# Optimization experiments

Measured on AMD Instinct MI355X. Metric: run time of the kernel, lower is better.

## Reference

```python
import jax, jax.numpy as jnp
import numpy as np
from jax import lax

N_NODES = 20000
N_EDGES = 320000
FEAT = 100
N_RULES = 64
T_RULE = 50
H_RNN = 256
RULE_NUMS = 16
NTN_OUT = 200


def setup_inputs() -> dict:
    key = jax.random.key(0)
    ks = iter(jax.random.split(key, 64))
    nrm = lambda shape, s=0.05: jax.random.normal(next(ks), shape, jnp.float32) * s
    inp = {}
    inp["node_features_0"] = jax.random.normal(next(ks), (N_NODES, FEAT), jnp.float32)
    inp["node_features_1"] = jax.random.normal(next(ks), (N_NODES, FEAT), jnp.float32)
    inp["edge_indices_0"] = jax.random.randint(next(ks), (2, N_EDGES), 0, N_NODES)
    inp["edge_indices_1"] = jax.random.randint(next(ks), (2, N_EDGES), 0, N_NODES)
    inp["edge_features_0"] = jax.random.normal(next(ks), (N_EDGES, FEAT), jnp.float32)
    inp["edge_features_1"] = jax.random.normal(next(ks), (N_EDGES, FEAT), jnp.float32)
    inp["rules"] = jax.random.normal(next(ks), (N_RULES, T_RULE, FEAT), jnp.float32)
    # TripleConv 1: edge lin (3*100 -> 100) and nn = mlp (100->100->100)
    inp["c1_lin_W"] = nrm((FEAT, 3 * FEAT)); inp["c1_lin_b"] = jnp.zeros((FEAT,))
    inp["c1_W1"] = nrm((FEAT, FEAT)); inp["c1_b1"] = jnp.zeros((FEAT,))
    inp["c1_W2"] = nrm((FEAT, FEAT)); inp["c1_b2"] = jnp.zeros((FEAT,))
    # TripleConv 2
    inp["c2_lin_W"] = nrm((FEAT, 3 * FEAT)); inp["c2_lin_b"] = jnp.zeros((FEAT,))
    inp["c2_W1"] = nrm((FEAT, FEAT)); inp["c2_b1"] = jnp.zeros((FEAT,))
    inp["c2_W2"] = nrm((FEAT, FEAT)); inp["c2_b2"] = jnp.zeros((FEAT,))
    # NTN (input_dim=100 to match pooled graph vectors, out_dim=200)
    inp["ntn_W"] = nrm((FEAT, FEAT, NTN_OUT))
    inp["ntn_V"] = nrm((NTN_OUT, 2 * FEAT))
    inp["ntn_B"] = jnp.zeros((NTN_OUT,))
    # RuleEmbedding: 2-layer tanh RNN (100 -> 256 -> 256) + Linear(256,100)
    inp["rnn0_Wih"] = nrm((H_RNN, FEAT)); inp["rnn0_Whh"] = nrm((H_RNN, H_RNN))
    inp["rnn0_bih"] = jnp.zeros((H_RNN,)); inp["rnn0_bhh"] = jnp.zeros((H_RNN,))
    inp["rnn1_Wih"] = nrm((H_RNN, H_RNN)); inp["rnn1_Whh"] = nrm((H_RNN, H_RNN))
    inp["rnn1_bih"] = jnp.zeros((H_RNN,)); inp["rnn1_bhh"] = jnp.zeros((H_RNN,))
    inp["rule_lin_W"] = nrm((FEAT, H_RNN)); inp["rule_lin_b"] = jnp.zeros((FEAT,))
    # RuleRanker 100->128->64->1
    inp["rk_W1"] = nrm((128, FEAT)); inp["rk_b1"] = jnp.zeros((128,))
    inp["rk_W2"] = nrm((64, 128)); inp["rk_b2"] = jnp.zeros((64,))
    inp["rk_W3"] = nrm((1, 64)); inp["rk_b3"] = jnp.zeros((1,))
    # Head: fc1 (200 + rule_nums*100 -> 500) -> fc2 (500->100) -> fc3 (100->1)
    inp["fc1_W"] = nrm((500, NTN_OUT + RULE_NUMS * FEAT)); inp["fc1_b"] = jnp.zeros((500,))
    inp["fc2_W"] = nrm((FEAT, 500)); inp["fc2_b"] = jnp.zeros((FEAT,))
    inp["fc3_W"] = nrm((1, FEAT)); inp["fc3_b"] = jnp.zeros((1,))
    return inp


def _triple_conv(x, src, dst, e, lin_W, lin_b, W1, b1, W2, b2):
    # message: relu(Linear(concat(x_i, edge_attr, x_j))); PyG: i=target, j=source
    m = jax.nn.relu(jnp.concatenate([x[dst], e, x[src]], axis=1) @ lin_W.T + lin_b)
    agg = jax.ops.segment_sum(m, dst, num_segments=x.shape[0])  # aggr='add'
    out = agg + x  # (1 + eps) * x_r with eps = 0
    h = jax.nn.relu(out @ W1.T + b1)
    return h @ W2.T + b2  # nn = Sequential(Linear, ReLU, Linear)


def _conv_pass(x, ei, e, c_lin_W, c_lin_b, c_W1, c_b1, c_W2, c_b2,
               d_lin_W, d_lin_b, d_W1, d_b1, d_W2, d_b2):
    src, dst = ei[0], ei[1]
    x = jax.nn.relu(_triple_conv(x, src, dst, e, c_lin_W, c_lin_b, c_W1, c_b1, c_W2, c_b2))
    x = jax.nn.relu(_triple_conv(x, src, dst, e, d_lin_W, d_lin_b, d_W1, d_b1, d_W2, d_b2))
    return x


def _rnn_layer(x_tbf, Wih, Whh, bih, bhh):
    # x_tbf: [T, B, in]; returns all hidden states [T, B, H] and final [B, H]
    h0 = jnp.zeros((x_tbf.shape[1], Whh.shape[0]), x_tbf.dtype)
    def step(h, xt):
        h = jnp.tanh(xt @ Wih.T + bih + h @ Whh.T + bhh)
        return h, h
    hT, ys = lax.scan(step, h0, x_tbf)
    return ys, hT


def reference(node_features_0, node_features_1, edge_indices_0, edge_indices_1,
              edge_features_0, edge_features_1, rules,
              c1_lin_W, c1_lin_b, c1_W1, c1_b1, c1_W2, c1_b2,
              c2_lin_W, c2_lin_b, c2_W1, c2_b1, c2_W2, c2_b2,
              ntn_W, ntn_V, ntn_B,
              rnn0_Wih, rnn0_Whh, rnn0_bih, rnn0_bhh,
              rnn1_Wih, rnn1_Whh, rnn1_bih, rnn1_bhh,
              rule_lin_W, rule_lin_b,
              rk_W1, rk_b1, rk_W2, rk_b2, rk_W3, rk_b3,
              fc1_W, fc1_b, fc2_W, fc2_b, fc3_W, fc3_b):
    # --- rule embedding (all sequences full length => pack/pad is identity) ---
    x = jnp.transpose(rules, (1, 0, 2))  # [T, B, 100]
    ys, _ = _rnn_layer(x, rnn0_Wih, rnn0_Whh, rnn0_bih, rnn0_bhh)
    _, hT = _rnn_layer(ys, rnn1_Wih, rnn1_Whh, rnn1_bih, rnn1_bhh)
    rules_embedding = hT @ rule_lin_W.T + rule_lin_b  # [B, 100]
    # --- rule ranking + top-k ---
    h = jax.nn.relu(rules_embedding @ rk_W1.T + rk_b1)
    h = jax.nn.relu(h @ rk_W2.T + rk_b2)
    rules_score = jax.nn.sigmoid(h @ rk_W3.T + rk_b3)[:, 0]  # [B]
    _, top_idx = lax.top_k(rules_score, RULE_NUMS)
    top_rules_embedding = rules_embedding[top_idx]  # [rule_nums, 100]
    # --- GNN message passing on both graphs ---
    f1 = _conv_pass(node_features_0, edge_indices_0, edge_features_0,
                    c1_lin_W, c1_lin_b, c1_W1, c1_b1, c1_W2, c1_b2,
                    c2_lin_W, c2_lin_b, c2_W1, c2_b1, c2_W2, c2_b2)
    f2 = _conv_pass(node_features_1, edge_indices_1, edge_features_1,
                    c1_lin_W, c1_lin_b, c1_W1, c1_b1, c1_W2, c1_b2,
                    c2_lin_W, c2_lin_b, c2_W1, c2_b1, c2_W2, c2_b2)
    g1 = jnp.sum(f1, axis=0, keepdims=True)  # global_add_pool, single graph -> [1, 100]
    g2 = jnp.sum(f2, axis=0, keepdims=True)
    # --- NTN(g1, g2) ---
    tp = jnp.einsum('ai,ijk,bj->abk', g1, ntn_W, g2)  # [1,1,200]
    concat = jnp.concatenate([g1[:, None, :] * jnp.ones_like(g2)[None, :, :1],
                              g2[None, :, :] * jnp.ones_like(g1)[:, None, :1]], axis=2)
    lin_term = concat @ ntn_V.T  # [1,1,200]
    ntn_out = jax.nn.relu(tp + lin_term + ntn_B).reshape(-1)  # squeeze -> [200]
    # --- scoring head ---
    feat = jnp.concatenate([ntn_out, top_rules_embedding.reshape(-1)])  # [200 + rule_nums*100]
    z = jax.nn.relu(feat @ fc1_W.T + fc1_b)
    z = jax.nn.relu(z @ fc2_W.T + fc2_b)
    score = jax.nn.sigmoid(z @ fc3_W.T + fc3_b)
    return score.reshape(())
```

## Files before the change

### kernel.cpp

```cpp
#include <hip/hip_runtime.h>

typedef unsigned short u16;
typedef unsigned int u32;

#define N_NODES 20000
#define N_EDGES 320000
#define FEAT 100
#define XPAD 112
#define N_RULES 64
#define T_RULE 50
#define H_RNN 256
#define RULE_NUMS 16
#define NTN_OUT 200
#define SCAN_B 79
#define NPB 16

typedef __attribute__((ext_vector_type(8))) short short8;
typedef __attribute__((ext_vector_type(4))) float f32x4;

__device__ __forceinline__ u16 f2bu(float f) {
  u32 u = __float_as_uint(f);
  u32 r = (u + 0x7fffu + ((u >> 16) & 1u)) >> 16;
  return (u16)r;
}
__device__ __forceinline__ float bu2f(u16 u) {
  return __uint_as_float(((u32)u) << 16);
}
__device__ __forceinline__ u32 pk2(float a, float b) {
  return (u32)f2bu(a) | ((u32)f2bu(b) << 16);
}

__device__ __forceinline__ void lds_st16(void* base, int byteOff, uint4 v) {
  *(uint4*)((char*)base + byteOff) = v;
}
__device__ __forceinline__ short8 lds_ld16(const void* base, int byteOff) {
  return *(const short8*)((const char*)base + byteOff);
}

#define SWZ(row, kByte) (((((row) << 8) + (kByte))) ^ (((row) & 7) << 4))

__device__ __forceinline__ int hs_off(int row, int chunk) {
  return (row << 9) | (((chunk + row * 5) & 31) << 4);
}

__device__ __forceinline__ float tanh_fast(float x) {
  const float e = __expf(2.f * x);
  return 1.f - 2.f / (e + 1.f);
}

__global__ void k_prep(const float* __restrict__ nf0, const float* __restrict__ nf1,
                       u16* __restrict__ xb0, u16* __restrict__ xb1) {
  const int total = N_NODES * XPAD;
  for (int i = blockIdx.x * blockDim.x + threadIdx.x; i < total;
       i += gridDim.x * blockDim.x) {
    const int n = i / XPAD;
    const int c = i - n * XPAD;
    const float v0 = (c < FEAT) ? nf0[(size_t)n * FEAT + c] : 0.f;
    const float v1 = (c < FEAT) ? nf1[(size_t)n * FEAT + c] : 0.f;
    xb0[i] = f2bu(v0);
    xb1[i] = f2bu(v1);
  }
}

__global__ void k_wprep(const float* __restrict__ linW, u16* __restrict__ Wb) {
  const int idx = blockIdx.x * blockDim.x + threadIdx.x;
  if (idx >= 3 * 128 * 128) return;
  const int c = idx >> 14;
  const int rem = idx & 16383;
  const int r = rem >> 7;
  const int k = rem & 127;
  u16 v = 0;
  if (r < FEAT && k < FEAT) v = f2bu(linW[(size_t)r * 300 + c * 100 + k]);
  Wb[idx] = v;
}

__global__ void k_wprep_sq(const float* __restrict__ W, u16* __restrict__ Wb) {
  const int idx = blockIdx.x * blockDim.x + threadIdx.x;
  if (idx >= 128 * 128) return;
  const int r = idx >> 7;
  const int k = idx & 127;
  u16 v = 0;
  if (r < FEAT && k < FEAT) v = f2bu(W[(size_t)r * FEAT + k]);
  Wb[idx] = v;
}

__global__ void k_count2(const int* __restrict__ d0, const int* __restrict__ d1,
                         int* __restrict__ cnt) {
  const int e = blockIdx.x * blockDim.x + threadIdx.x;
  const int* d = blockIdx.y ? d1 : d0;
  if (e < N_EDGES) atomicAdd(&cnt[blockIdx.y * N_NODES + d[e]], 1);
}

__global__ __launch_bounds__(256) void k_scan1(const int* __restrict__ cnt,
                                               int* __restrict__ off,
                                               int* __restrict__ bsum) {
  __shared__ int buf[256];
  const int g = blockIdx.y, b = blockIdx.x, tid = threadIdx.x;
  const int i = b * 256 + tid;
  const int v = (i < N_NODES) ? cnt[g * N_NODES + i] : 0;
  buf[tid] = v;
  __syncthreads();
  for (int ofs = 1; ofs < 256; ofs <<= 1) {
    const int t = (tid >= ofs) ? buf[tid - ofs] : 0;
    __syncthreads();
    buf[tid] += t;
    __syncthreads();
  }
  if (i < N_NODES) off[g * (N_NODES + 1) + i] = buf[tid] - v;
  if (tid == 255) bsum[g * SCAN_B + b] = buf[255];
}

__global__ __launch_bounds__(128) void k_scan2(int* __restrict__ bsum) {
  __shared__ int s[128];
  const int g = blockIdx.y, tid = threadIdx.x;
  const int v = (tid < SCAN_B) ? bsum[g * SCAN_B + tid] : 0;
  s[tid] = v;
  __syncthreads();
  for (int ofs = 1; ofs < 128; ofs <<= 1) {
    const int t = (tid >= ofs) ? s[tid - ofs] : 0;
    __syncthreads();
    s[tid] += t;
    __syncthreads();
  }
  if (tid < SCAN_B) bsum[g * SCAN_B + tid] = s[tid] - v;
}

__global__ __launch_bounds__(256) void k_scan3(const int* __restrict__ bsum,
                                               int* __restrict__ off,
                                               int* __restrict__ cursor) {
  const int g = blockIdx.y, b = blockIdx.x, tid = threadIdx.x;
  const int i = b * 256 + tid;
  if (i < N_NODES) {
    const int o = off[g * (N_NODES + 1) + i] + bsum[g * SCAN_B + b];
    off[g * (N_NODES + 1) + i] = o;
    cursor[g * N_NODES + i] = o;
  }
  if (i == N_NODES) off[g * (N_NODES + 1) + N_NODES] = N_EDGES;
}

__global__ void k_scatter2(const int* __restrict__ s0, const int* __restrict__ d0,
                           const int* __restrict__ s1, const int* __restrict__ d1,
                           int* __restrict__ cursor,
                           int* __restrict__ el0, int* __restrict__ el1,
                           int* __restrict__ sp0, int* __restrict__ sp1,
                           int* __restrict__ dp0, int* __restrict__ dp1) {
  const int e = blockIdx.x * blockDim.x + threadIdx.x;
  const int g = blockIdx.y;
  const int* d = g ? d1 : d0;
  const int* s = g ? s1 : s0;
  if (e < N_EDGES) {
    const int dn = d[e];
    const int pos = atomicAdd(&cursor[g * N_NODES + dn], 1);
    (g ? el1 : el0)[pos] = e;
    (g ? sp1 : sp0)[pos] = s[e];
    (g ? dp1 : dp0)[pos] = dn;
  }
}

template <int VARIANT>
__global__ __launch_bounds__(256) void k_gemm_u(
    const float* __restrict__ Af, const u16* __restrict__ Ab,
    const float* __restrict__ W, const float* __restrict__ b0,
    const float* __restrict__ b1, float* __restrict__ Uout) {
  __shared__ __align__(16) u16 As[64 * 128];
  __shared__ __align__(16) u16 Bs[128 * 128];
  const int tid = threadIdx.x;
  const int lane = tid & 63;
  const int wv = tid >> 6;
  const int l15 = lane & 15;
  const int lhi = lane >> 4;
  const int mb = blockIdx.x * 64;
  const int nb = blockIdx.y * 128;
  const int rb = (wv >> 1) * 32;
  const int cb = (wv & 1) * 64;
  constexpr int KV = VARIANT ? 256 : 100;
  constexpr int NPH = VARIANT ? 2 : 1;

  f32x4 acc[2][4];
  const f32x4 z4 = {0.f, 0.f, 0.f, 0.f};
#pragma unroll
  for (int i = 0; i < 2; ++i)
#pragma unroll
    for (int j = 0; j < 4; ++j) acc[i][j] = z4;

  for (int kc = 0; kc < NPH; ++kc) {
    __syncthreads();
    {
      const int row = tid >> 2;
      const int k0 = (tid & 3) * 32;
      const int gm = mb + row;
      if (VARIANT == 0) {
        const int r = gm & 63;
        const int t = gm >> 6;
        const float* ar = Af + ((size_t)r * T_RULE + t) * FEAT;
#pragma unroll
        for (int c = 0; c < 4; ++c) {
          const int k = k0 + c * 8;
          uint4 v = {0u, 0u, 0u, 0u};
          if (k + 8 <= KV) {
            const float4 fa = *(const float4*)(ar + k);
            const float4 fb = *(const float4*)(ar + k + 4);
            v.x = pk2(fa.x, fa.y); v.y = pk2(fa.z, fa.w);
            v.z = pk2(fb.x, fb.y); v.w = pk2(fb.z, fb.w);
          } else if (k < KV) {
            const float4 fa = *(const float4*)(ar + k);
            v.x = pk2(fa.x, fa.y); v.y = pk2(fa.z, fa.w);
          }
          lds_st16(As, SWZ(row, k * 2), v);
        }
      } else {
        const uint4* ar = (const uint4*)(Ab + (size_t)gm * 256 + kc * 128 + k0);
#pragma unroll
        for (int c = 0; c < 4; ++c)
          lds_st16(As, SWZ(row, (k0 + c * 8) * 2), ar[c]);
      }
    }
    {
      const int row = tid >> 1;
      const int k0 = (tid & 1) * 64;
      const float* wr = W + (size_t)(nb + row) * KV;
#pragma unroll
      for (int c = 0; c < 8; ++c) {
        const int k = k0 + c * 8;
        const int kg = kc * 128 + k;
        uint4 v = {0u, 0u, 0u, 0u};
        if (kg + 8 <= KV) {
          const float4 fa = *(const float4*)(wr + kg);
          const float4 fb = *(const float4*)(wr + kg + 4);
          v.x = pk2(fa.x, fa.y); v.y = pk2(fa.z, fa.w);
          v.z = pk2(fb.x, fb.y); v.w = pk2(fb.z, fb.w);
        } else if (kg < KV) {
          const float4 fa = *(const float4*)(wr + kg);
          v.x = pk2(fa.x, fa.y); v.y = pk2(fa.z, fa.w);
        }
        lds_st16(Bs, SWZ(row, k * 2), v);
      }
    }
    __syncthreads();
#pragma unroll
    for (int s = 0; s < 4; ++s) {
      const int kByte = s * 64 + lhi * 16;
      short8 af[2], bfr[4];
#pragma unroll
      for (int i = 0; i < 2; ++i)
        af[i] = lds_ld16(As, SWZ(rb + i * 16 + l15, kByte));
#pragma unroll
      for (int j = 0; j < 4; ++j)
        bfr[j] = lds_ld16(Bs, SWZ(cb + j * 16 + l15, kByte));
#pragma unroll
      for (int i = 0; i < 2; ++i)
#pragma unroll
        for (int j = 0; j < 4; ++j)
          acc[i][j] = __builtin_amdgcn_mfma_f32_16x16x32_bf16(af[i], bfr[j],
                                                              acc[i][j], 0, 0, 0);
    }
  }
#pragma unroll
  for (int j = 0; j < 4; ++j) {
    const int col = nb + cb + j * 16 + l15;
    const float bias = b0[col] + b1[col];
#pragma unroll
    for (int i = 0; i < 2; ++i) {
      const int base_m = mb + rb + i * 16 + lhi * 4;
      const int t = base_m >> 6;
      const int r0 = base_m & 63;
      float4 st;
      st.x = acc[i][j][0] + bias; st.y = acc[i][j][1] + bias;
      st.z = acc[i][j][2] + bias; st.w = acc[i][j][3] + bias;
      *(float4*)(Uout + ((size_t)t * 256 + col) * 64 + r0) = st;
    }
  }
}

template <int WRITE_YS>
__global__ __launch_bounds__(512) void k_rec(
    const float* __restrict__ U, const float* __restrict__ Whh,
    u16* __restrict__ ys, float* __restrict__ hT) {
  __shared__ __align__(16) u16 Hs[16 * 256];
  const int tid = threadIdx.x;
  const int lane = tid & 63;
  const int wv = tid >> 6;
  const int cbase = wv * 32;
  const int ruleBase = blockIdx.x * 16;
  const int l15 = lane & 15;
  const int lhi = lane >> 4;

  short8 bf[2][8];
#pragma unroll
  for (int jt = 0; jt < 2; ++jt) {
    const int col = cbase + jt * 16 + l15;
    const float* wr = Whh + (size_t)col * 256;
#pragma unroll
    for (int s = 0; s < 8; ++s) {
      const int k0 = s * 32 + lhi * 8;
      const float4 fa = *(const float4*)(wr + k0);
      const float4 fb = *(const float4*)(wr + k0 + 4);
      uint4 v;
      v.x = pk2(fa.x, fa.y); v.y = pk2(fa.z, fa.w);
      v.z = pk2(fb.x, fb.y); v.w = pk2(fb.z, fb.w);
      bf[jt][s] = *(short8*)&v;
    }
  }
  for (int i = tid; i < 16 * 256 / 8; i += 512) {
    const uint4 z = {0u, 0u, 0u, 0u};
    ((uint4*)Hs)[i] = z;
  }
  __syncthreads();

  const int n0 = cbase + l15;
  const int n1 = cbase + 16 + l15;
  const int m0 = lhi * 4;
  float4 Ua0 = *(const float4*)(U + ((size_t)n0) * 64 + m0);
  float4 Ua1 = *(const float4*)(U + ((size_t)n1) * 64 + m0);

  const f32x4 z4 = {0.f, 0.f, 0.f, 0.f};
  float hv[2][4];
  for (int t = 0; t < T_RULE; ++t) {
    const int tn = (t + 1 < T_RULE) ? t + 1 : t;
    const float4 Ub0 = *(const float4*)(U + ((size_t)tn * 256 + n0) * 64 + m0);
    const float4 Ub1 = *(const float4*)(U + ((size_t)tn * 256 + n1) * 64 + m0);
    f32x4 acc[2] = {z4, z4};
#pragma unroll
    for (int s = 0; s < 8; ++s) {
      const short8 af = lds_ld16(Hs, hs_off(l15, s * 4 + lhi));
      acc[0] = __builtin_amdgcn_mfma_f32_16x16x32_bf16(af, bf[0][s], acc[0], 0, 0, 0);
      acc[1] = __builtin_amdgcn_mfma_f32_16x16x32_bf16(af, bf[1][s], acc[1], 0, 0, 0);
    }
    const float ua0[4] = {Ua0.x, Ua0.y, Ua0.z, Ua0.w};
    const float ua1[4] = {Ua1.x, Ua1.y, Ua1.z, Ua1.w};
#pragma unroll
    for (int q = 0; q < 4; ++q) {
      hv[0][q] = tanh_fast(ua0[q] + acc[0][q]);
      hv[1][q] = tanh_fast(ua1[q] + acc[1][q]);
    }
    __syncthreads();
#pragma unroll
    for (int jt = 0; jt < 2; ++jt) {
      const int n = cbase + jt * 16 + l15;
#pragma unroll
      for (int q = 0; q < 4; ++q) {
        const int m = lhi * 4 + q;
        const u16 hb = f2bu(hv[jt][q]);
        *(u16*)((char*)Hs + (hs_off(m, n >> 3) + ((n & 7) << 1))) = hb;
        if (WRITE_YS)
          ys[(((size_t)t * 64 + ruleBase + m) << 8) + n] = hb;
      }
    }
    Ua0 = Ub0; Ua1 = Ub1;
    __syncthreads();
  }
  if (!WRITE_YS) {
#pragma unroll
    for (int jt = 0; jt < 2; ++jt) {
      const int n = cbase + jt * 16 + l15;
#pragma unroll
      for (int q = 0; q < 4; ++q) {
        const int m = lhi * 4 + q;
        hT[((size_t)(ruleBase + m) << 8) + n] = hv[jt][q];
      }
    }
  }
}

__global__ __launch_bounds__(128) void k_rulelin(
    const float* __restrict__ hT, const float* __restrict__ rlW,
    const float* __restrict__ rlb, float* __restrict__ emb) {
  __shared__ __align__(16) float hs[H_RNN];
  const int b = blockIdx.x;
  const int tid = threadIdx.x;
  for (int i = tid; i < H_RNN / 4; i += 128)
    ((float4*)hs)[i] = ((const float4*)(hT + (size_t)b * H_RNN))[i];
  __syncthreads();
  if (tid < FEAT) {
    float acc = rlb[tid];
    const float4* w = (const float4*)(rlW + (size_t)tid * H_RNN);
    const float4* hv = (const float4*)hs;
#pragma unroll 8
    for (int k = 0; k < 64; ++k) {
      const float4 a = w[k], x = hv[k];
      acc += a.x * x.x + a.y * x.y + a.z * x.z + a.w * x.w;
    }
    emb[(size_t)b * FEAT + tid] = acc;
  }
}

__global__ __launch_bounds__(128) void k_ranker(
    const float* __restrict__ emb,
    const float* __restrict__ W1, const float* __restrict__ b1,
    const float* __restrict__ W2, const float* __restrict__ b2,
    const float* __restrict__ W3, const float* __restrict__ b3,
    float* __restrict__ scores) {
  __shared__ float eb[FEAT];
  __shared__ float h1s[128];
  __shared__ float h2s[64];
  const int r = blockIdx.x;
  const int tid = threadIdx.x;
  if (tid < FEAT) eb[tid] = emb[(size_t)r * FEAT + tid];
  __syncthreads();
  {
    float acc = b1[tid];
    const float* w = W1 + (size_t)tid * FEAT;
    for (int k = 0; k < FEAT; ++k) acc += w[k] * eb[k];
    h1s[tid] = acc > 0.f ? acc : 0.f;
  }
  __syncthreads();
  if (tid < 64) {
    float acc = b2[tid];
    const float* w = W2 + (size_t)tid * 128;
    for (int k = 0; k < 128; ++k) acc += w[k] * h1s[k];
    h2s[tid] = acc > 0.f ? acc : 0.f;
  }
  __syncthreads();
  if (tid == 0) {
    float acc = b3[0];
    for (int k = 0; k < 64; ++k) acc += W3[k] * h2s[k];
    scores[r] = acc;
  }
}

__global__ void k_topk(const float* __restrict__ scores, int* __restrict__ topidx) {
  if (threadIdx.x == 0 && blockIdx.x == 0) {
    float s[N_RULES];
    for (int i = 0; i < N_RULES; ++i) s[i] = scores[i];
    for (int t = 0; t < RULE_NUMS; ++t) {
      int best = 0;
      float bv = s[0];
      for (int i = 1; i < N_RULES; ++i)
        if (s[i] > bv) { bv = s[i]; best = i; }
      topidx[t] = best;
      s[best] = -1e30f;
    }
  }
}

__global__ __launch_bounds__(256) void k_nodegemm(
    const u16* __restrict__ xb, const u16* __restrict__ Wb,
    const float* __restrict__ linB, u16* __restrict__ P, u16* __restrict__ Q) {
  __shared__ __align__(16) u16 As[128 * 128];
  __shared__ __align__(16) u16 Bs[128 * 128];
  const int tid = threadIdx.x;
  const int lane = tid & 63;
  const int wv = tid >> 6;
  const int l15 = lane & 15;
  const int lhi = lane >> 4;
  const int n0 = blockIdx.x * 128;
  const int p = blockIdx.y;
  const int rStage = tid >> 1;
  const int hf = tid & 1;
  const int rb = (wv >> 1) * 64;
  const int cb = (wv & 1) * 64;

  {
    const int node = n0 + rStage;
    const bool ok = node < N_NODES;
    const uint4* xr = (const uint4*)(xb + (size_t)node * XPAD);
#pragma unroll
    for (int q = 0; q < 8; ++q) {
      const int cc = hf * 8 + q;
      uint4 v = {0u, 0u, 0u, 0u};
      if (ok && cc < 14) v = xr[cc];
      lds_st16(As, SWZ(rStage, cc * 16), v);
    }
  }
  {
    const uint4* wr = (const uint4*)(Wb + (size_t)(p ? 2 : 0) * 16384 +
                                     (size_t)rStage * 128);
#pragma unroll
    for (int q = 0; q < 8; ++q) {
      const int cc = hf * 8 + q;
      lds_st16(Bs, SWZ(rStage, cc * 16), wr[cc]);
    }
  }
  __syncthreads();

  f32x4 acc[4][4];
  const f32x4 z4 = {0.f, 0.f, 0.f, 0.f};
#pragma unroll
  for (int i = 0; i < 4; ++i)
#pragma unroll
    for (int j = 0; j < 4; ++j) acc[i][j] = z4;
#pragma unroll
  for (int s = 0; s < 4; ++s) {
    const int kByte = s * 64 + lhi * 16;
    short8 af[4], bfr[4];
#pragma unroll
    for (int i = 0; i < 4; ++i) {
      af[i] = lds_ld16(As, SWZ(rb + i * 16 + l15, kByte));
      bfr[i] = lds_ld16(Bs, SWZ(cb + i * 16 + l15, kByte));
    }
#pragma unroll
    for (int i = 0; i < 4; ++i)
#pragma unroll
      for (int j = 0; j < 4; ++j)
        acc[i][j] = __builtin_amdgcn_mfma_f32_16x16x32_bf16(af[i], bfr[j],
                                                            acc[i][j], 0, 0, 0);
  }
  u16* Out = p ? Q : P;
#pragma unroll
  for (int j = 0; j < 4; ++j) {
    const int col = cb + j * 16 + l15;
    if (col >= XPAD) continue;
    const bool valid = col < FEAT;
    const float bias = (valid && !p) ? linB[col] : 0.f;
#pragma unroll
    for (int i = 0; i < 4; ++i) {
      const int row0 = rb + i * 16 + lhi * 4;
#pragma unroll
      for (int q = 0; q < 4; ++q) {
        const int node = n0 + row0 + q;
        if (node < N_NODES)
          Out[(size_t)node * XPAD + col] = valid ? f2bu(acc[i][j][q] + bias) : (u16)0;
      }
    }
  }
}

__global__ __launch_bounds__(256, 3) void k_msgagg2(
    const float* __restrict__ ef, const u16* __restrict__ Wb,
    const int* __restrict__ elist, const int* __restrict__ spos,
    const int* __restrict__ dpos, const int* __restrict__ off,
    const u16* __restrict__ Pb, const u16* __restrict__ Qb,
    const u16* __restrict__ xb, u16* __restrict__ aggb) {
  __shared__ __align__(16) u16 As[64 * 128];
  const int tid = threadIdx.x;
  const int lane = tid & 63;
  const int wv = tid >> 6;
  const int l15 = lane & 15;
  const int lhi = lane >> 4;
  const int nb0 = blockIdx.x * NPB;
  const int rr = tid >> 2;
  const int t4 = tid & 3;
  const int cb = wv * 32;
  const f32x4 z4 = {0.f, 0.f, 0.f, 0.f};

  const int p0 = off[nb0];
  const int pEnd = off[nb0 + NPB];

  const int sl = tid >> 4;
  const int sc8 = tid & 15;
  const int myS = off[nb0 + sl];
  const int myE = off[nb0 + sl + 1];
  float a8[8] = {0.f, 0.f, 0.f, 0.f, 0.f, 0.f, 0.f, 0.f};

  short8 bf[2][4];
  {
    const u16* wbase = Wb + 16384;
#pragma unroll
    for (int jt = 0; jt < 2; ++jt) {
      const u16* wr = wbase + (size_t)(cb + jt * 16 + l15) * 128;
#pragma unroll
      for (int s = 0; s < 4; ++s)
        bf[jt][s] = *(const short8*)(wr + s * 32 + lhi * 8);
    }
  }

  for (int base = p0; base < pEnd; base += 64) {
    const int slot = base + rr;
    const bool valid = slot < pEnd;
    {
      const int e = valid ? elist[slot] : 0;
      const int k0 = t4 * 32;
      const float* ar = ef + (size_t)e * FEAT;
#pragma unroll
      for (int c = 0; c < 4; ++c) {
        const int k = k0 + c * 8;
        uint4 v = {0u, 0u, 0u, 0u};
        if (valid) {
          if (k + 8 <= FEAT) {
            const float4 fa = *(const float4*)(ar + k);
            const float4 fb = *(const float4*)(ar + k + 4);
            v.x = pk2(fa.x, fa.y); v.y = pk2(fa.z, fa.w);
            v.z = pk2(fb.x, fb.y); v.w = pk2(fb.z, fb.w);
          } else if (k < FEAT) {
            const float4 fa = *(const float4*)(ar + k);
            v.x = pk2(fa.x, fa.y); v.y = pk2(fa.z, fa.w);
          }
        }
        lds_st16(As, SWZ(rr, k * 2), v);
      }
    }
    __syncthreads();
    f32x4 acc[4][2];
#pragma unroll
    for (int i = 0; i < 4; ++i)
#pragma unroll
      for (int j = 0; j < 2; ++j) acc[i][j] = z4;
#pragma unroll
    for (int s = 0; s < 4; ++s) {
      const int kByte = s * 64 + lhi * 16;
      short8 af[4];
#pragma unroll
      for (int i = 0; i < 4; ++i)
        af[i] = lds_ld16(As, SWZ(i * 16 + l15, kByte));
#pragma unroll
      for (int i = 0; i < 4; ++i)
#pragma unroll
        for (int j = 0; j < 2; ++j)
          acc[i][j] = __builtin_amdgcn_mfma_f32_16x16x32_bf16(af[i], bf[j][s],
                                                              acc[i][j], 0, 0, 0);
    }
    __syncthreads();
#pragma unroll
    for (int i = 0; i < 4; ++i) {
#pragma unroll
      for (int j = 0; j < 2; ++j) {
        const int col = cb + j * 16 + l15;
#pragma unroll
        for (int q = 0; q < 4; ++q) {
          const int row = i * 16 + lhi * 4 + q;
          *(u16*)((char*)As + (SWZ(row, col * 2))) = f2bu(acc[i][j][q]);
        }
      }
    }
    __syncthreads();
    {
      const int dn = valid ? dpos[slot] : 0;
      const int sn = valid ? spos[slot] : 0;
#pragma unroll
      for (int c = 0; c < 4; ++c) {
        const int chunk = t4 * 4 + c;
        if (chunk >= 14) break;
        const uint4 p4 = *(const uint4*)(Pb + (size_t)dn * XPAD + chunk * 8);
        const uint4 q4 = *(const uint4*)(Qb + (size_t)sn * XPAD + chunk * 8);
        const short8 ev = lds_ld16(As, SWZ(rr, chunk * 16));
        const uint4 e4 = *(const uint4*)&ev;
        uint4 o;
        float v0 = bu2f((u16)(e4.x & 0xffffu)) + bu2f((u16)(p4.x & 0xffffu)) +
                   bu2f((u16)(q4.x & 0xffffu));
        float v1 = bu2f((u16)(e4.x >> 16)) + bu2f((u16)(p4.x >> 16)) +
                   bu2f((u16)(q4.x >> 16));
        o.x = pk2(v0 > 0.f ? v0 : 0.f, v1 > 0.f ? v1 : 0.f);
        float v2 = bu2f((u16)(e4.y & 0xffffu)) + bu2f((u16)(p4.y & 0xffffu)) +
                   bu2f((u16)(q4.y & 0xffffu));
        float v3 = bu2f((u16)(e4.y >> 16)) + bu2f((u16)(p4.y >> 16)) +
                   bu2f((u16)(q4.y >> 16));
        o.y = pk2(v2 > 0.f ? v2 : 0.f, v3 > 0.f ? v3 : 0.f);
        float v4 = bu2f((u16)(e4.z & 0xffffu)) + bu2f((u16)(p4.z & 0xffffu)) +
                   bu2f((u16)(q4.z & 0xffffu));
        float v5 = bu2f((u16)(e4.z >> 16)) + bu2f((u16)(p4.z >> 16)) +
                   bu2f((u16)(q4.z >> 16));
        o.z = pk2(v4 > 0.f ? v4 : 0.f, v5 > 0.f ? v5 : 0.f);
        float v6 = bu2f((u16)(e4.w & 0xffffu)) + bu2f((u16)(p4.w & 0xffffu)) +
                   bu2f((u16)(q4.w & 0xffffu));
        float v7 = bu2f((u16)(e4.w >> 16)) + bu2f((u16)(p4.w >> 16)) +
                   bu2f((u16)(q4.w >> 16));
        o.w = pk2(v6 > 0.f ? v6 : 0.f, v7 > 0.f ? v7 : 0.f);
        lds_st16(As, SWZ(rr, chunk * 16), o);
      }
    }
    __syncthreads();
    {
      const int gs = myS > base ? myS : base;
      const int ge = myE < base + 64 ? myE : base + 64;
      for (int r = gs; r < ge; ++r) {
        const short8 mv = lds_ld16(As, SWZ(r - base, sc8 * 16));
        const uint4 m4 = *(const uint4*)&mv;
        a8[0] += bu2f((u16)(m4.x & 0xffffu)); a8[1] += bu2f((u16)(m4.x >> 16));
        a8[2] += bu2f((u16)(m4.y & 0xffffu)); a8[3] += bu2f((u16)(m4.y >> 16));
        a8[4] += bu2f((u16)(m4.z & 0xffffu)); a8[5] += bu2f((u16)(m4.z >> 16));
        a8[6] += bu2f((u16)(m4.w & 0xffffu)); a8[7] += bu2f((u16)(m4.w >> 16));
      }
    }
    __syncthreads();
  }
  if (sc8 < 14) {
    const int node = nb0 + sl;
    const uint4 xv = *(const uint4*)(xb + (size_t)node * XPAD + sc8 * 8);
    uint4 o;
    o.x = pk2(a8[0] + bu2f((u16)(xv.x & 0xffffu)),
              a8[1] + bu2f((u16)(xv.x >> 16)));
    o.y = pk2(a8[2] + bu2f((u16)(xv.y & 0xffffu)),
              a8[3] + bu2f((u16)(xv.y >> 16)));
    o.z = pk2(a8[4] + bu2f((u16)(xv.z & 0xffffu)),
              a8[5] + bu2f((u16)(xv.z >> 16)));
    o.w = pk2(a8[6] + bu2f((u16)(xv.w & 0xffffu)),
              a8[7] + bu2f((u16)(xv.w >> 16)));
    *(uint4*)(aggb + (size_t)node * XPAD + sc8 * 8) = o;
  }
}

__global__ __launch_bounds__(256) void k_mlp(
    const u16* __restrict__ aggb, const u16* __restrict__ W1b,
    const float* __restrict__ b1, const u16* __restrict__ W2b,
    const float* __restrict__ b2, u16* __restrict__ xbout) {
  __shared__ __align__(16) u16 As[128 * 128];
  __shared__ __align__(16) u16 Bs[128 * 128];
  const int tid = threadIdx.x;
  const int lane = tid & 63;
  const int wv = tid >> 6;
  const int l15 = lane & 15;
  const int lhi = lane >> 4;
  const int n0 = blockIdx.x * 128;
  const int rStage = tid >> 1;
  const int hf = tid & 1;
  const int rb = (wv >> 1) * 64;
  const int cb = (wv & 1) * 64;
  const f32x4 z4 = {0.f, 0.f, 0.f, 0.f};

  {
    const int node = n0 + rStage;
    const bool ok = node < N_NODES;
    const uint4* xr = (const uint4*)(aggb + (size_t)node * XPAD);
#pragma unroll
    for (int q = 0; q < 8; ++q) {
      const int cc = hf * 8 + q;
      uint4 v = {0u, 0u, 0u, 0u};
      if (ok && cc < 14) v = xr[cc];
      lds_st16(As, SWZ(rStage, cc * 16), v);
    }
  }
  {
    const uint4* wr = (const uint4*)(W1b + (size_t)rStage * 128);
#pragma unroll
    for (int q = 0; q < 8; ++q) {
      const int cc = hf * 8 + q;
      lds_st16(Bs, SWZ(rStage, cc * 16), wr[cc]);
    }
  }
  __syncthreads();

  f32x4 acc[4][4];
#pragma unroll
  for (int i = 0; i < 4; ++i)
#pragma unroll
    for (int j = 0; j < 4; ++j) acc[i][j] = z4;
#pragma unroll
  for (int s = 0; s < 4; ++s) {
    const int kByte = s * 64 + lhi * 16;
    short8 af[4], bfr[4];
#pragma unroll
    for (int i = 0; i < 4; ++i) {
      af[i] = lds_ld16(As, SWZ(rb + i * 16 + l15, kByte));
      bfr[i] = lds_ld16(Bs, SWZ(cb + i * 16 + l15, kByte));
    }
#pragma unroll
    for (int i = 0; i < 4; ++i)
#pragma unroll
      for (int j = 0; j < 4; ++j)
        acc[i][j] = __builtin_amdgcn_mfma_f32_16x16x32_bf16(af[i], bfr[j],
                                                            acc[i][j], 0, 0, 0);
  }
  __syncthreads();
#pragma unroll
  for (int j = 0; j < 4; ++j) {
    const int col = cb + j * 16 + l15;
    const float bias = (col < FEAT) ? b1[col] : 0.f;
#pragma unroll
    for (int i = 0; i < 4; ++i) {
      const int row0 = rb + i * 16 + lhi * 4;
#pragma unroll
      for (int q = 0; q < 4; ++q) {
        float v = acc[i][j][q] + bias;
        v = v > 0.f ? v : 0.f;
        *(u16*)((char*)As + (SWZ(row0 + q, col * 2))) = f2bu(v);
      }
    }
  }
  {
    const uint4* wr = (const uint4*)(W2b + (size_t)rStage * 128);
#pragma unroll
    for (int q = 0; q < 8; ++q) {
      const int cc = hf * 8 + q;
      lds_st16(Bs, SWZ(rStage, cc * 16), wr[cc]);
    }
  }
  __syncthreads();

#pragma unroll
  for (int i = 0; i < 4; ++i)
#pragma unroll
    for (int j = 0; j < 4; ++j) acc[i][j] = z4;
#pragma unroll
  for (int s = 0; s < 4; ++s) {
    const int kByte = s * 64 + lhi * 16;
    short8 af[4], bfr[4];
#pragma unroll
    for (int i = 0; i < 4; ++i) {
      af[i] = lds_ld16(As, SWZ(rb + i * 16 + l15, kByte));
      bfr[i] = lds_ld16(Bs, SWZ(cb + i * 16 + l15, kByte));
    }
#pragma unroll
    for (int i = 0; i < 4; ++i)
#pragma unroll
      for (int j = 0; j < 4; ++j)
        acc[i][j] = __builtin_amdgcn_mfma_f32_16x16x32_bf16(af[i], bfr[j],
                                                            acc[i][j], 0, 0, 0);
  }
#pragma unroll
  for (int j = 0; j < 4; ++j) {
    const int col = cb + j * 16 + l15;
    if (col >= XPAD) continue;
    const bool valid = col < FEAT;
    const float bias = valid ? b2[col] : 0.f;
#pragma unroll
    for (int i = 0; i < 4; ++i) {
      const int row0 = rb + i * 16 + lhi * 4;
#pragma unroll
      for (int q = 0; q < 4; ++q) {
        const int node = n0 + row0 + q;
        if (node < N_NODES) {
          float v = acc[i][j][q] + bias;
          v = v > 0.f ? v : 0.f;
          xbout[(size_t)node * XPAD + col] = valid ? f2bu(v) : (u16)0;
        }
      }
    }
  }
}

__global__ void k_pool(const u16* __restrict__ xb, float* __restrict__ g) {
  const int tid = threadIdx.x;
  if (tid >= FEAT) return;
  float s = 0.f;
  const int n0 = blockIdx.x * 100;
  for (int i = 0; i < 100; ++i) s += bu2f(xb[(size_t)(n0 + i) * XPAD + tid]);
  atomicAdd(&g[tid], s);
}

__global__ __launch_bounds__(256) void k_ntn(const float* __restrict__ W,
                                             const float* __restrict__ g1,
                                             const float* __restrict__ g2,
                                             float* __restrict__ tp) {
  __shared__ float g2s[FEAT];
  const int i = blockIdx.x;
  const int tid = threadIdx.x;
  if (tid < FEAT) g2s[tid] = g2[tid];
  __syncthreads();
  if (tid < NTN_OUT) {
    const float g1i = g1[i];
    float acc = 0.f;
    const float* wr = W + (size_t)i * FEAT * NTN_OUT + tid;
    for (int jj = 0; jj < FEAT; ++jj) acc += wr[(size_t)jj * NTN_OUT] * g2s[jj];
    atomicAdd(&tp[tid], g1i * acc);
  }
}

__global__ __launch_bounds__(256) void k_feat(
    const float* __restrict__ tp, const float* __restrict__ gv,
    const float* __restrict__ V, const float* __restrict__ B,
    const float* __restrict__ emb, const int* __restrict__ topidx,
    float* __restrict__ featOut) {
  const int tid = threadIdx.x;
  if (tid < NTN_OUT) {
    float acc = B[tid] + tp[tid];
    const float* vr = V + (size_t)tid * 200;
    for (int k = 0; k < 200; ++k) acc += vr[k] * gv[k];
    featOut[tid] = acc > 0.f ? acc : 0.f;
  }
  for (int i = tid; i < RULE_NUMS * FEAT; i += 256) {
    const int rr = i / FEAT;
    const int cc = i - rr * FEAT;
    featOut[NTN_OUT + i] = emb[(size_t)topidx[rr] * FEAT + cc];
  }
}

__global__ __launch_bounds__(256) void k_fc1(
    const float* __restrict__ feat, const float* __restrict__ W,
    const float* __restrict__ b, float* __restrict__ z1) {
  __shared__ __align__(16) float fs[NTN_OUT + RULE_NUMS * FEAT];
  const int tid = threadIdx.x;
  for (int i = tid; i < 450; i += 256) ((float4*)fs)[i] = ((const float4*)feat)[i];
  __syncthreads();
  const int lane = tid & 63;
  const int wv = tid >> 6;
  const int o = blockIdx.x * 4 + wv;
  float acc = 0.f;
  const float4* w4 = (const float4*)(W + (size_t)o * 1800);
  const float4* f4 = (const float4*)fs;
  for (int k = lane; k < 450; k += 64) {
    const float4 a = w4[k], x = f4[k];
    acc += a.x * x.x + a.y * x.y + a.z * x.z + a.w * x.w;
  }
#pragma unroll
  for (int d = 32; d; d >>= 1) acc += __shfl_down(acc, d);
  if (lane == 0) {
    acc += b[o];
    z1[o] = acc > 0.f ? acc : 0.f;
  }
}

__global__ __launch_bounds__(128) void k_head2(
    const float* __restrict__ z1g, const float* __restrict__ fc2W,
    const float* __restrict__ fc2b, const float* __restrict__ fc3W,
    const float* __restrict__ fc3b, float* __restrict__ out) {
  __shared__ __align__(16) float z1[500];
  __shared__ float z2[FEAT];
  const int tid = threadIdx.x;
  for (int i = tid; i < 125; i += 128) ((float4*)z1)[i] = ((const float4*)z1g)[i];
  __syncthreads();
  if (tid < FEAT) {
    float acc = fc2b[tid];
    const float4* w4 = (const float4*)(fc2W + (size_t)tid * 500);
    const float4* f4 = (const float4*)z1;
#pragma unroll 5
    for (int k = 0; k < 125; ++k) {
      const float4 a = w4[k], x = f4[k];
      acc += a.x * x.x + a.y * x.y + a.z * x.z + a.w * x.w;
    }
    z2[tid] = acc > 0.f ? acc : 0.f;
  }
  __syncthreads();
  if (tid == 0) {
    float acc = fc3b[0];
    for (int k = 0; k < FEAT; ++k) acc += fc3W[k] * z2[k];
    out[0] = 1.f / (1.f + expf(-acc));
  }
}

extern "C" void kernel_launch(void* const* d_in, const int* in_sizes, int n_in,
                              void* d_out, int out_size, void* d_ws, size_t ws_size,
                              hipStream_t stream) {
  (void)in_sizes; (void)n_in; (void)out_size; (void)ws_size;

  const float* nf[2] = {(const float*)d_in[0], (const float*)d_in[1]};
  const int* ei[2] = {(const int*)d_in[2], (const int*)d_in[3]};
  const float* ef[2] = {(const float*)d_in[4], (const float*)d_in[5]};
  const float* rules = (const float*)d_in[6];
  const float* cw[2][6];
  for (int l = 0; l < 2; ++l)
    for (int k = 0; k < 6; ++k) cw[l][k] = (const float*)d_in[7 + l * 6 + k];
  const float* ntnW = (const float*)d_in[19];
  const float* ntnV = (const float*)d_in[20];
  const float* ntnB = (const float*)d_in[21];
  const float* r0Wih = (const float*)d_in[22];
  const float* r0Whh = (const float*)d_in[23];
  const float* r0bih = (const float*)d_in[24];
  const float* r0bhh = (const float*)d_in[25];
  const float* r1Wih = (const float*)d_in[26];
  const float* r1Whh = (const float*)d_in[27];
  const float* r1bih = (const float*)d_in[28];
  const float* r1bhh = (const float*)d_in[29];
  const float* rlW = (const float*)d_in[30];
  const float* rlb = (const float*)d_in[31];
  const float* rkW1 = (const float*)d_in[32];
  const float* rkb1 = (const float*)d_in[33];
  const float* rkW2 = (const float*)d_in[34];
  const float* rkb2 = (const float*)d_in[35];
  const float* rkW3 = (const float*)d_in[36];
  const float* rkb3 = (const float*)d_in[37];
  const float* fc1W = (const float*)d_in[38];
  const float* fc1b = (const float*)d_in[39];
  const float* fc2W = (const float*)d_in[40];
  const float* fc2b = (const float*)d_in[41];
  const float* fc3W = (const float*)d_in[42];
  const float* fc3b = (const float*)d_in[43];

  char* base = (char*)d_ws;
  size_t woff = 0;
#define WS_ALLOC(T, NAME, BYTES) \
  T* NAME = (T*)(base + woff);   \
  woff = (woff + (size_t)(BYTES) + 255) & ~(size_t)255;
  WS_ALLOC(char, rnn_buf, (size_t)5242880)
  WS_ALLOC(u16, xb0, (size_t)N_NODES * XPAD * 2)
  WS_ALLOC(u16, xb1, (size_t)N_NODES * XPAD * 2)
  WS_ALLOC(u16, Pbuf, (size_t)N_NODES * XPAD * 2)
  WS_ALLOC(u16, Qbuf, (size_t)N_NODES * XPAD * 2)
  WS_ALLOC(u16, aggb, (size_t)N_NODES * XPAD * 2)
  WS_ALLOC(u16, Wb0, (size_t)3 * 128 * 128 * 2)
  WS_ALLOC(u16, Wb1, (size_t)3 * 128 * 128 * 2)
  WS_ALLOC(u16, Wm, (size_t)4 * 128 * 128 * 2)
  WS_ALLOC(int, offAll, (size_t)2 * (N_NODES + 1) * 4)
  WS_ALLOC(int, cursor, (size_t)2 * N_NODES * 4)
  WS_ALLOC(int, bsum, (size_t)2 * SCAN_B * 4)
  WS_ALLOC(int, el0, (size_t)N_EDGES * 4)
  WS_ALLOC(int, el1, (size_t)N_EDGES * 4)
  WS_ALLOC(int, sp0, (size_t)N_EDGES * 4)
  WS_ALLOC(int, sp1, (size_t)N_EDGES * 4)
  WS_ALLOC(int, dp0, (size_t)N_EDGES * 4)
  WS_ALLOC(int, dp1, (size_t)N_EDGES * 4)
  WS_ALLOC(float, emb, (size_t)N_RULES * FEAT * 4)
  WS_ALLOC(float, scores, (size_t)N_RULES * 4)
  WS_ALLOC(int, topidx, (size_t)RULE_NUMS * 4)
  WS_ALLOC(float, gtp, (size_t)(2 * FEAT + NTN_OUT) * 4)
#undef WS_ALLOC
  u16* xb[2] = {xb0, xb1};
  int* elg[2] = {el0, el1};
  int* spg[2] = {sp0, sp1};
  int* dpg[2] = {dp0, dp1};
  u16* Wbl[2] = {Wb0, Wb1};
  float* gv = gtp;
  float* tp = gtp + 200;

  float* U   = (float*)rnn_buf;
  u16*   ys  = (u16*)(rnn_buf + 3276800);
  float* hT  = (float*)(rnn_buf + 4915200);
  float* featWS = (float*)(rnn_buf + 4980736);
  float* z1WS   = (float*)(rnn_buf + 4988160);

  hipMemsetAsync(cursor, 0, (size_t)2 * N_NODES * 4, stream);
  hipMemsetAsync(gtp, 0, (size_t)(2 * FEAT + NTN_OUT) * 4, stream);

  k_prep<<<2048, 256, 0, stream>>>(nf[0], nf[1], xb[0], xb[1]);
  k_wprep<<<192, 256, 0, stream>>>(cw[0][0], Wb0);
  k_wprep<<<192, 256, 0, stream>>>(cw[1][0], Wb1);
  k_wprep_sq<<<64, 256, 0, stream>>>(cw[0][2], Wm);
  k_wprep_sq<<<64, 256, 0, stream>>>(cw[0][4], Wm + 16384);
  k_wprep_sq<<<64, 256, 0, stream>>>(cw[1][2], Wm + 2 * 16384);
  k_wprep_sq<<<64, 256, 0, stream>>>(cw[1][4], Wm + 3 * 16384);

  const int* src0 = ei[0];
  const int* src1 = ei[1];
  const int* dst0 = ei[0] + N_EDGES;
  const int* dst1 = ei[1] + N_EDGES;
  k_count2<<<dim3(1250, 2), 256, 0, stream>>>(dst0, dst1, cursor);
  k_scan1<<<dim3(SCAN_B, 2), 256, 0, stream>>>(cursor, offAll, bsum);
  k_scan2<<<dim3(1, 2), 128, 0, stream>>>(bsum);
  k_scan3<<<dim3(SCAN_B, 2), 256, 0, stream>>>(bsum, offAll, cursor);
  k_scatter2<<<dim3(1250, 2), 256, 0, stream>>>(src0, dst0, src1, dst1, cursor,
                                                el0, el1, sp0, sp1, dp0, dp1);

  {
    dim3 gg(50, 2);
    k_gemm_u<0><<<gg, 256, 0, stream>>>(rules, nullptr, r0Wih, r0bih, r0bhh, U);
    k_rec<1><<<4, 512, 0, stream>>>(U, r0Whh, ys, nullptr);
    k_gemm_u<1><<<gg, 256, 0, stream>>>(nullptr, ys, r1Wih, r1bih, r1bhh, U);
    k_rec<0><<<4, 512, 0, stream>>>(U, r1Whh, nullptr, hT);
    k_rulelin<<<N_RULES, 128, 0, stream>>>(hT, rlW, rlb, emb);
  }
  k_ranker<<<N_RULES, 128, 0, stream>>>(emb, rkW1, rkb1, rkW2, rkb2, rkW3, rkb3,
                                        scores);
  k_topk<<<1, 64, 0, stream>>>(scores, topidx);

  for (int g = 0; g < 2; ++g) {
    const int* offg = offAll + g * (N_NODES + 1);
    for (int l = 0; l < 2; ++l) {
      k_nodegemm<<<dim3(157, 2), 256, 0, stream>>>(xb[g], Wbl[l], cw[l][1],
                                                   Pbuf, Qbuf);
      k_msgagg2<<<N_NODES / NPB, 256, 0, stream>>>(ef[g], Wbl[l], elg[g], spg[g],
                                                   dpg[g], offg, Pbuf, Qbuf,
                                                   xb[g], aggb);
      k_mlp<<<157, 256, 0, stream>>>(aggb, Wm + (size_t)(2 * l) * 16384, cw[l][3],
                                     Wm + (size_t)(2 * l + 1) * 16384, cw[l][5],
                                     xb[g]);
    }
    k_pool<<<200, 128, 0, stream>>>(xb[g], gv + g * FEAT);
  }

  k_ntn<<<FEAT, 256, 0, stream>>>(ntnW, gv, gv + FEAT, tp);
  k_feat<<<1, 256, 0, stream>>>(tp, gv, ntnV, ntnB, emb, topidx, featWS);
  k_fc1<<<125, 256, 0, stream>>>(featWS, fc1W, fc1b, z1WS);
  k_head2<<<1, 128, 0, stream>>>(z1WS, fc2W, fc2b, fc3W, fc3b, (float*)d_out);
}
```

Before: 842.5 us.

## Batch both graphs into single launches per conv layer

Merges the per-graph loops so each conv layer launches nodegemm, msgagg2 and mlp once with an extra grid dimension covering both graphs. Separate P/Q/agg buffers are allocated per graph. This cuts the number of kernel launches and doubles grid size, which should help fill the GPU on small kernels like k_mlp with 157 blocks. msgagg2 launch bounds also rise from 3 to 4 blocks per CU, which may raise register pressure or cause spills.

```diff
diff --git a/kernel.cpp b/kernel.cpp
--- a/kernel.cpp
+++ b/kernel.cpp
@@ -434,8 +434,10 @@
 }
 
 __global__ __launch_bounds__(256) void k_nodegemm(
-    const u16* __restrict__ xb, const u16* __restrict__ Wb,
-    const float* __restrict__ linB, u16* __restrict__ P, u16* __restrict__ Q) {
+    const u16* __restrict__ xbA, const u16* __restrict__ xbB,
+    const u16* __restrict__ Wb, const float* __restrict__ linB,
+    u16* __restrict__ PA, u16* __restrict__ QA,
+    u16* __restrict__ PB, u16* __restrict__ QB) {
   __shared__ __align__(16) u16 As[128 * 128];
   __shared__ __align__(16) u16 Bs[128 * 128];
   const int tid = threadIdx.x;
@@ -445,6 +447,9 @@
   const int lhi = lane >> 4;
   const int n0 = blockIdx.x * 128;
   const int p = blockIdx.y;
+  const int gph = blockIdx.z;
+  const u16* xb = gph ? xbB : xbA;
+  u16* Out = gph ? (p ? QB : PB) : (p ? QA : PA);
   const int rStage = tid >> 1;
   const int hf = tid & 1;
   const int rb = (wv >> 1) * 64;
@@ -495,7 +500,6 @@
         acc[i][j] = __builtin_amdgcn_mfma_f32_16x16x32_bf16(af[i], bfr[j],
                                                             acc[i][j], 0, 0, 0);
   }
-  u16* Out = p ? Q : P;
 #pragma unroll
   for (int j = 0; j < 4; ++j) {
     const int col = cb + j * 16 + l15;
@@ -515,13 +519,29 @@
   }
 }
 
-__global__ __launch_bounds__(256, 3) void k_msgagg2(
-    const float* __restrict__ ef, const u16* __restrict__ Wb,
-    const int* __restrict__ elist, const int* __restrict__ spos,
-    const int* __restrict__ dpos, const int* __restrict__ off,
-    const u16* __restrict__ Pb, const u16* __restrict__ Qb,
-    const u16* __restrict__ xb, u16* __restrict__ aggb) {
+__global__ __launch_bounds__(256, 4) void k_msgagg2(
+    const float* __restrict__ efA, const float* __restrict__ efB,
+    const u16* __restrict__ Wb,
+    const int* __restrict__ elA, const int* __restrict__ elB,
+    const int* __restrict__ spA, const int* __restrict__ spB,
+    const int* __restrict__ dpA, const int* __restrict__ dpB,
+    const int* __restrict__ offAll,
+    const u16* __restrict__ PA, const u16* __restrict__ QA,
+    const u16* __restrict__ PB, const u16* __restrict__ QB,
+    const u16* __restrict__ xbA, const u16* __restrict__ xbB,
+    u16* __restrict__ aggA, u16* __restrict__ aggB) {
   __shared__ __align__(16) u16 As[64 * 128];
+  const int gph = blockIdx.y;
+  const float* ef = gph ? efB : efA;
+  const int* elist = gph ? elB : elA;
+  const int* spos = gph ? spB : spA;
+  const int* dpos = gph ? dpB : dpA;
+  const int* off = offAll + gph * (N_NODES + 1);
+  const u16* Pb = gph ? PB : PA;
+  const u16* Qb = gph ? QB : QA;
+  const u16* xb = gph ? xbB : xbA;
+  u16* aggb = gph ? aggB : aggA;
+
   const int tid = threadIdx.x;
   const int lane = tid & 63;
   const int wv = tid >> 6;
@@ -680,11 +700,15 @@
 }
 
 __global__ __launch_bounds__(256) void k_mlp(
-    const u16* __restrict__ aggb, const u16* __restrict__ W1b,
-    const float* __restrict__ b1, const u16* __restrict__ W2b,
-    const float* __restrict__ b2, u16* __restrict__ xbout) {
+    const u16* __restrict__ aggA, const u16* __restrict__ aggB,
+    const u16* __restrict__ W1b, const float* __restrict__ b1,
+    const u16* __restrict__ W2b, const float* __restrict__ b2,
+    u16* __restrict__ xbA, u16* __restrict__ xbB) {
   __shared__ __align__(16) u16 As[128 * 128];
   __shared__ __align__(16) u16 Bs[128 * 128];
+  const int gph = blockIdx.y;
+  const u16* aggb = gph ? aggB : aggA;
+  u16* xbout = gph ? xbB : xbA;
   const int tid = threadIdx.x;
   const int lane = tid & 63;
   const int wv = tid >> 6;
@@ -953,9 +977,12 @@
   WS_ALLOC(char, rnn_buf, (size_t)5242880)
   WS_ALLOC(u16, xb0, (size_t)N_NODES * XPAD * 2)
   WS_ALLOC(u16, xb1, (size_t)N_NODES * XPAD * 2)
-  WS_ALLOC(u16, Pbuf, (size_t)N_NODES * XPAD * 2)
-  WS_ALLOC(u16, Qbuf, (size_t)N_NODES * XPAD * 2)
-  WS_ALLOC(u16, aggb, (size_t)N_NODES * XPAD * 2)
+  WS_ALLOC(u16, Pbuf0, (size_t)N_NODES * XPAD * 2)
+  WS_ALLOC(u16, Qbuf0, (size_t)N_NODES * XPAD * 2)
+  WS_ALLOC(u16, Pbuf1, (size_t)N_NODES * XPAD * 2)
+  WS_ALLOC(u16, Qbuf1, (size_t)N_NODES * XPAD * 2)
+  WS_ALLOC(u16, aggb0, (size_t)N_NODES * XPAD * 2)
+  WS_ALLOC(u16, aggb1, (size_t)N_NODES * XPAD * 2)
   WS_ALLOC(u16, Wb0, (size_t)3 * 128 * 128 * 2)
   WS_ALLOC(u16, Wb1, (size_t)3 * 128 * 128 * 2)
   WS_ALLOC(u16, Wm, (size_t)4 * 128 * 128 * 2)
@@ -974,9 +1001,6 @@
   WS_ALLOC(float, gtp, (size_t)(2 * FEAT + NTN_OUT) * 4)
 #undef WS_ALLOC
   u16* xb[2] = {xb0, xb1};
-  int* elg[2] = {el0, el1};
-  int* spg[2] = {sp0, sp1};
-  int* dpg[2] = {dp0, dp1};
   u16* Wbl[2] = {Wb0, Wb1};
   float* gv = gtp;
   float* tp = gtp + 200;
@@ -1021,20 +1045,19 @@
                                         scores);
   k_topk<<<1, 64, 0, stream>>>(scores, topidx);
 
-  for (int g = 0; g < 2; ++g) {
-    const int* offg = offAll + g * (N_NODES + 1);
-    for (int l = 0; l < 2; ++l) {
-      k_nodegemm<<<dim3(157, 2), 256, 0, stream>>>(xb[g], Wbl[l], cw[l][1],
-                                                   Pbuf, Qbuf);
-      k_msgagg2<<<N_NODES / NPB, 256, 0, stream>>>(ef[g], Wbl[l], elg[g], spg[g],
-                                                   dpg[g], offg, Pbuf, Qbuf,
-                                                   xb[g], aggb);
-      k_mlp<<<157, 256, 0, stream>>>(aggb, Wm + (size_t)(2 * l) * 16384, cw[l][3],
-                                     Wm + (size_t)(2 * l + 1) * 16384, cw[l][5],
-                                     xb[g]);
-    }
-    k_pool<<<200, 128, 0, stream>>>(xb[g], gv + g * FEAT);
-  }
+  for (int l = 0; l < 2; ++l) {
+    k_nodegemm<<<dim3(157, 2, 2), 256, 0, stream>>>(xb0, xb1, Wbl[l], cw[l][1],
+                                                    Pbuf0, Qbuf0, Pbuf1, Qbuf1);
+    k_msgagg2<<<dim3(N_NODES / NPB, 2), 256, 0, stream>>>(
+        ef[0], ef[1], Wbl[l], el0, el1, sp0, sp1, dp0, dp1, offAll,
+        Pbuf0, Qbuf0, Pbuf1, Qbuf1, xb0, xb1, aggb0, aggb1);
+    k_mlp<<<dim3(157, 2), 256, 0, stream>>>(aggb0, aggb1,
+                                            Wm + (size_t)(2 * l) * 16384, cw[l][3],
+                                            Wm + (size_t)(2 * l + 1) * 16384,
+                                            cw[l][5], xb0, xb1);
+  }
+  k_pool<<<200, 128, 0, stream>>>(xb0, gv);
+  k_pool<<<200, 128, 0, stream>>>(xb1, gv + FEAT);
 
   k_ntn<<<FEAT, 256, 0, stream>>>(ntnW, gv, gv + FEAT, tp);
   k_feat<<<1, 256, 0, stream>>>(tp, gv, ntnV, ntnB, emb, topidx, featWS);
```

Result: slower. 963.8 us (+14.4%).
